# Kernel tuning notes

Hardware: AMD Instinct MI355X
Metric: run time of the kernel (lower is better)

The kernel has to match this reference:

```python
import jax, jax.numpy as jnp
import numpy as np
from jax import lax

STRIDE = 2
PADDING = 2
EPS = 1e-5


def _conv1d(x, w):
    # x: (N, C_in, T), w: (C_out, C_in, K) -> (N, C_out, T_out)
    return lax.conv_general_dilated(
        x, w, window_strides=(STRIDE,), padding=[(PADDING, PADDING)],
        dimension_numbers=("NCH", "OIH", "NCH"))


def setup_inputs() -> dict:
    key = jax.random.key(0)
    ks = jax.random.split(key, 5)
    Batch, num_sensors, in_c, out_c, k, T, r = 32, 8, 64, 128, 5, 2048, 8
    x = jax.random.normal(ks[0], (Batch * num_sensors, in_c, T), dtype=jnp.float32)
    A_flat = jax.random.normal(ks[1], (Batch, r * in_c * k), dtype=jnp.float32) * 0.02
    B_flat = jax.random.normal(ks[2], (Batch, out_c * r), dtype=jnp.float32) * 0.02
    fan_in = in_c * k
    conv_w = jax.random.normal(ks[3], (out_c, in_c, k), dtype=jnp.float32) / np.sqrt(fan_in)
    conv_b = jax.random.normal(ks[4], (out_c,), dtype=jnp.float32) * 0.01
    gamma = jnp.ones((out_c,), dtype=jnp.float32)
    beta = jnp.zeros((out_c,), dtype=jnp.float32)
    return {"x": x, "A_flat": A_flat, "B_flat": B_flat,
            "conv_w": conv_w, "conv_b": conv_b, "gamma": gamma, "beta": beta,
            "num_sensors": num_sensors, "r": r, "lora_scale": 0.5}


def reference(x, A_flat, B_flat, conv_w, conv_b, gamma, beta, num_sensors, r, lora_scale):
    Batch = A_flat.shape[0]
    out_c, in_c, k = conv_w.shape
    T = x.shape[-1]

    # base conv1d
    out_base = _conv1d(x, conv_w) + conv_b[None, :, None]  # (B*S, out_c, T_out)

    # dynamic per-sample LoRA delta weight: delta_W = B @ A, (Batch, out_c, in_c, k)
    A = A_flat.reshape(Batch, r, in_c * k)
    B_mat = B_flat.reshape(Batch, out_c, r)
    delta_W = jnp.einsum("bor,brm->bom", B_mat, A).reshape(Batch, out_c, in_c, k)
    delta_W = delta_W * lora_scale

    # per-sample conv: sensors of one sample share that sample's delta weight
    x_b = x.reshape(Batch, num_sensors, in_c, T)
    lora_out = jax.vmap(_conv1d)(x_b, delta_W)  # (Batch, S, out_c, T_out)
    lora_out = lora_out.reshape(Batch * num_sensors, out_c, -1)

    out = jax.nn.relu(out_base + lora_out)

    # GroupNorm, num_groups = min(4, out_c) reduced until divisible
    G = min(4, out_c)
    while out_c % G != 0:
        G -= 1
    N, C, To = out.shape
    og = out.reshape(N, G, C // G, To)
    mean = og.mean(axis=(2, 3), keepdims=True)
    var = og.var(axis=(2, 3), keepdims=True)
    normed = ((og - mean) * lax.rsqrt(var + EPS)).reshape(N, C, To)
    return normed * gamma[None, :, None] + beta[None, :, None]
```

## Files before the change

### kernel.cpp

```cpp
#include <hip/hip_runtime.h>
#include <hip/hip_bf16.h>

#define EPSV 1e-5f
#define PITCH 36
#define PCOLS 516

typedef short bf16x8 __attribute__((ext_vector_type(8)));
typedef short bf16x4 __attribute__((ext_vector_type(4)));
typedef float f32x4  __attribute__((ext_vector_type(4)));

__device__ __forceinline__ short f2bf(float f){
  unsigned u = __float_as_uint(f);
  u += 0x7fff + ((u >> 16) & 1);
  return (short)(u >> 16);
}
__device__ __forceinline__ int pk2(float a, float b){
  __hip_bfloat162 h = __float22bfloat162_rn(float2{a, b});
  return *reinterpret_cast<int*>(&h);
}

__global__ void build_weights(const float* __restrict__ A_flat,
                              const float* __restrict__ B_flat,
                              const float* __restrict__ conv_w,
                              const float* __restrict__ scale_p,
                              short* __restrict__ Wb){
  int idx = blockIdx.x * 256 + threadIdx.x;
  int ci = idx & 63;
  int co = (idx >> 6) & 127;
  int bj = idx >> 13;
  int b  = bj / 5;
  int j  = bj - 5 * b;
  int m  = ci * 5 + j;
  const float* Bp = B_flat + (b * 128 + co) * 8;
  const float* Ap = A_flat + b * 8 * 320 + m;
  float d = 0.f;
#pragma unroll
  for (int r = 0; r < 8; ++r) d = fmaf(Bp[r], Ap[r * 320], d);
  float w = conv_w[co * 320 + m] + scale_p[0] * d;
  Wb[idx] = f2bf(w);
}

__global__ __launch_bounds__(512, 4)
void conv_gn_mfma(const float* __restrict__ x,
                  const short* __restrict__ Wb,
                  const float* __restrict__ conv_b,
                  const float* __restrict__ gamma,
                  const float* __restrict__ beta,
                  float* __restrict__ out){
  __shared__ short xe[PCOLS * PITCH];
  __shared__ short xo[PCOLS * PITCH];
  __shared__ float redS[8], redQ[8], bc2[2];

  const int bid    = blockIdx.x;
  const int sample = ((bid & 7) << 5) + (bid >> 5);
  const int g      = (bid >> 3) & 3;
  const int b      = sample >> 3;
  const int tid    = threadIdx.x;
  const int lane   = tid & 63;
  const int wid    = tid >> 6;
  const int l16    = lane & 15;
  const int lk     = lane >> 4;

  f32x4 acc[2][8];
#pragma unroll
  for (int m2 = 0; m2 < 2; ++m2)
#pragma unroll
    for (int n = 0; n < 8; ++n) acc[m2][n] = (f32x4){0.f,0.f,0.f,0.f};

  const size_t wb_base = (size_t)b * 5 * 128 * 64;
  const float* xsamp = x + (size_t)sample * 64 * 2048;

#pragma unroll
  for (int ph = 0; ph < 4; ++ph) {
    const int th = ph >> 1;
    const int ch = ph & 1;

    if (ph) __syncthreads();
    {
      const float* xbase = xsamp + (size_t)(ch * 32) * 2048;
      const float* xr = xbase + (size_t)(wid * 4) * 2048 + th * 1024;
#pragma unroll 2
      for (int pass = 0; pass < 8; ++pass) {
        int c0 = pass * 128 + lane * 2;
        float2 v0 = *(const float2*)(xr + 0 * 2048 + c0);
        float2 v1 = *(const float2*)(xr + 1 * 2048 + c0);
        float2 v2 = *(const float2*)(xr + 2 * 2048 + c0);
        float2 v3 = *(const float2*)(xr + 3 * 2048 + c0);
        int pcol = pass * 64 + lane + 1;
        int2 ev = { pk2(v0.x, v1.x), pk2(v2.x, v3.x) };
        int2 od = { pk2(v0.y, v1.y), pk2(v2.y, v3.y) };
        *(int2*)(xe + pcol * PITCH + wid * 4) = ev;
        *(int2*)(xo + pcol * PITCH + wid * 4) = od;
      }
      if (tid < 128) {
        int which = tid >> 5;
        int ci    = tid & 31;
        int xc    = th * 1024 + ((which < 2) ? (which - 2) : (1024 + (which & 1)));
        float v = (xc >= 0 && xc < 2048) ? xbase[(size_t)ci * 2048 + xc] : 0.f;
        short* arr = (which & 1) ? xo : xe;
        arr[((which < 2) ? 0 : 513) * PITCH + ci] = f2bf(v);
      }
    }
    __syncthreads();
#pragma unroll
    for (int j = 0; j < 5; ++j) {
      const short* apb = Wb + wb_base + (size_t)(j * 128 + g * 32) * 64 + ch * 32 + lk * 8;
      bf16x8 a0 = *(const bf16x8*)(apb + (size_t)l16 * 64);
      bf16x8 a1 = *(const bf16x8*)(apb + (size_t)(l16 + 16) * 64);
      const short* arr = (j & 1) ? xo : xe;
      const int joff = (j & 1) ? ((j - 1) >> 1) : (j >> 1);
#pragma unroll
      for (int nn = 0; nn < 4; ++nn) {
        int tloc = wid * 64 + nn * 16 + l16;
        const short* bp = arr + (tloc + joff) * PITCH + lk * 8;
        bf16x4 lo = *(const bf16x4*)bp;
        bf16x4 hi = *(const bf16x4*)(bp + 4);
        bf16x8 bfr = {lo[0],lo[1],lo[2],lo[3],hi[0],hi[1],hi[2],hi[3]};
        const int n = th * 4 + nn;
        acc[0][n] = __builtin_amdgcn_mfma_f32_16x16x32_bf16(a0, bfr, acc[0][n], 0, 0, 0);
        acc[1][n] = __builtin_amdgcn_mfma_f32_16x16x32_bf16(a1, bfr, acc[1][n], 0, 0, 0);
      }
    }
  }

  float cb_[2][4], ga_[2][4], be_[2][4];
#pragma unroll
  for (int m2 = 0; m2 < 2; ++m2)
#pragma unroll
    for (int r = 0; r < 4; ++r) {
      int co = g * 32 + m2 * 16 + lk * 4 + r;
      cb_[m2][r] = conv_b[co];
      ga_[m2][r] = gamma[co];
      be_[m2][r] = beta[co];
    }
  float s1 = 0.f, s2 = 0.f;
#pragma unroll
  for (int m2 = 0; m2 < 2; ++m2)
#pragma unroll
    for (int n = 0; n < 8; ++n)
#pragma unroll
      for (int r = 0; r < 4; ++r) {
        float v = acc[m2][n][r] + cb_[m2][r];
        v = v > 0.f ? v : 0.f;
        acc[m2][n][r] = v;
        s1 += v;
        s2 = fmaf(v, v, s2);
      }
#pragma unroll
  for (int off = 32; off; off >>= 1) {
    s1 += __shfl_down(s1, off);
    s2 += __shfl_down(s2, off);
  }
  if (lane == 0) { redS[wid] = s1; redQ[wid] = s2; }
  __syncthreads();
  if (tid == 0) {
    float a = 0.f, q = 0.f;
#pragma unroll
    for (int w = 0; w < 8; ++w) { a += redS[w]; q += redQ[w]; }
    float mean = a * (1.f / 32768.f);
    float var  = q * (1.f / 32768.f) - mean * mean;
    bc2[0] = mean;
    bc2[1] = rsqrtf(var + EPSV);
  }
  __syncthreads();
  const float mean = bc2[0], inv = bc2[1];
  float* ob = out + (size_t)sample * 128 * 1024;
#pragma unroll
  for (int m2 = 0; m2 < 2; ++m2)
#pragma unroll
    for (int r = 0; r < 4; ++r) {
      int co = g * 32 + m2 * 16 + lk * 4 + r;
      float aa = ga_[m2][r] * inv;
      float bb = be_[m2][r] - mean * aa;
      float* orow = ob + (size_t)co * 1024 + l16;
#pragma unroll
      for (int n = 0; n < 8; ++n) {
        int t = (n >> 2) * 512 + wid * 64 + (n & 3) * 16;
        orow[t] = acc[m2][n][r] * aa + bb;
      }
    }
}

extern "C" void kernel_launch(void* const* d_in, const int* in_sizes, int n_in,
                              void* d_out, int out_size, void* d_ws, size_t ws_size,
                              hipStream_t stream) {
  const float* x       = (const float*)d_in[0];
  const float* A_flat  = (const float*)d_in[1];
  const float* B_flat  = (const float*)d_in[2];
  const float* conv_w  = (const float*)d_in[3];
  const float* conv_b  = (const float*)d_in[4];
  const float* gamma   = (const float*)d_in[5];
  const float* beta    = (const float*)d_in[6];
  const float* scale_p = (const float*)d_in[9];

  float* out = (float*)d_out;
  short* Wb  = (short*)d_ws;

  build_weights<<<5120, 256, 0, stream>>>(A_flat, B_flat, conv_w, scale_p, Wb);
  conv_gn_mfma<<<1024, 512, 0, stream>>>(x, Wb, conv_b, gamma, beta, out);
}
```

Before: 106.4 us.

## Give each wave a private LDS input tile and drop block barriers

The shared x staging buffers are split into per-wave tiles, each holding that wave's 64 output positions plus halo columns. Each wave now loads, converts and consumes its own slice, so the two `__syncthreads` per phase are removed and waves can run out of step with each other. The phase order is also swapped so the channel half is the outer loop. In exchange, each wave loads its halo columns again, and the LDS footprint grows slightly.

Result: slower. 111.5 us (+4.8%).

```diff
diff --git a/kernel.cpp b/kernel.cpp
--- a/kernel.cpp
+++ b/kernel.cpp
@@ -3,7 +3,8 @@
 
 #define EPSV 1e-5f
 #define PITCH 36
-#define PCOLS 516
+#define TILE_SH (66 * PITCH)
+#define WTILE_SH (2 * TILE_SH)
 
 typedef short bf16x8 __attribute__((ext_vector_type(8)));
 typedef short bf16x4 __attribute__((ext_vector_type(4)));
@@ -47,8 +48,7 @@
                   const float* __restrict__ gamma,
                   const float* __restrict__ beta,
                   float* __restrict__ out){
-  __shared__ short xe[PCOLS * PITCH];
-  __shared__ short xo[PCOLS * PITCH];
+  __shared__ short xt[8 * WTILE_SH];
   __shared__ float redS[8], redQ[8], bc2[2];
 
   const int bid    = blockIdx.x;
@@ -61,6 +61,9 @@
   const int l16    = lane & 15;
   const int lk     = lane >> 4;
 
+  short* xe = xt + wid * WTILE_SH;
+  short* xo = xe + TILE_SH;
+
   f32x4 acc[2][8];
 #pragma unroll
   for (int m2 = 0; m2 < 2; ++m2)
@@ -72,36 +75,40 @@
 
 #pragma unroll
   for (int ph = 0; ph < 4; ++ph) {
-    const int th = ph >> 1;
-    const int ch = ph & 1;
-
-    if (ph) __syncthreads();
+    const int ch = ph >> 1;
+    const int th = ph & 1;
+    const int T0 = th * 512 + wid * 64;
+
+    const float* xb = xsamp + (size_t)(ch * 32) * 2048;
+
     {
-      const float* xbase = xsamp + (size_t)(ch * 32) * 2048;
-      const float* xr = xbase + (size_t)(wid * 4) * 2048 + th * 1024;
-#pragma unroll 2
-      for (int pass = 0; pass < 8; ++pass) {
-        int c0 = pass * 128 + lane * 2;
-        float2 v0 = *(const float2*)(xr + 0 * 2048 + c0);
-        float2 v1 = *(const float2*)(xr + 1 * 2048 + c0);
-        float2 v2 = *(const float2*)(xr + 2 * 2048 + c0);
-        float2 v3 = *(const float2*)(xr + 3 * 2048 + c0);
-        int pcol = pass * 64 + lane + 1;
+      const int c = 2 * T0 + 2 * (int)lane;
+#pragma unroll
+      for (int rg = 0; rg < 8; ++rg) {
+        const float* r = xb + (size_t)(rg * 4) * 2048 + c;
+        float2 v0 = *(const float2*)(r);
+        float2 v1 = *(const float2*)(r + 2048);
+        float2 v2 = *(const float2*)(r + 4096);
+        float2 v3 = *(const float2*)(r + 6144);
         int2 ev = { pk2(v0.x, v1.x), pk2(v2.x, v3.x) };
         int2 od = { pk2(v0.y, v1.y), pk2(v2.y, v3.y) };
-        *(int2*)(xe + pcol * PITCH + wid * 4) = ev;
-        *(int2*)(xo + pcol * PITCH + wid * 4) = od;
-      }
-      if (tid < 128) {
-        int which = tid >> 5;
-        int ci    = tid & 31;
-        int xc    = th * 1024 + ((which < 2) ? (which - 2) : (1024 + (which & 1)));
-        float v = (xc >= 0 && xc < 2048) ? xbase[(size_t)ci * 2048 + xc] : 0.f;
-        short* arr = (which & 1) ? xo : xe;
-        arr[((which < 2) ? 0 : 513) * PITCH + ci] = f2bf(v);
-      }
-    }
-    __syncthreads();
+        *(int2*)(xe + (lane + 1) * PITCH + rg * 4) = ev;
+        *(int2*)(xo + (lane + 1) * PITCH + rg * 4) = od;
+      }
+      if (lane < 32) {
+        const int ci = lane;
+        float2 h{0.f, 0.f};
+        if (T0 > 0) h = *(const float2*)(xb + (size_t)ci * 2048 + (2 * T0 - 2));
+        xe[ci] = f2bf(h.x);
+        xo[ci] = f2bf(h.y);
+      } else {
+        const int ci = lane - 32;
+        const int xc = 2 * T0 + 128;
+        float v = (xc < 2048) ? xb[(size_t)ci * 2048 + xc] : 0.f;
+        xe[65 * PITCH + ci] = f2bf(v);
+      }
+    }
+
 #pragma unroll
     for (int j = 0; j < 5; ++j) {
       const short* apb = Wb + wb_base + (size_t)(j * 128 + g * 32) * 64 + ch * 32 + lk * 8;
@@ -111,8 +118,8 @@
       const int joff = (j & 1) ? ((j - 1) >> 1) : (j >> 1);
 #pragma unroll
       for (int nn = 0; nn < 4; ++nn) {
-        int tloc = wid * 64 + nn * 16 + l16;
-        const short* bp = arr + (tloc + joff) * PITCH + lk * 8;
+        int tl = nn * 16 + l16;
+        const short* bp = arr + (tl + joff) * PITCH + lk * 8;
         bf16x4 lo = *(const bf16x4*)bp;
         bf16x4 hi = *(const bf16x4*)(bp + 4);
         bf16x8 bfr = {lo[0],lo[1],lo[2],lo[3],hi[0],hi[1],hi[2],hi[3]};
```

## Double-buffer x tiles in LDS and compute two GroupNorm groups per block

Applied to the files above, without the earlier changes.

Each block now handles 64 output channels (two GroupNorm groups) rather than 32, which halves the grid and halves the number of times each sample's input is loaded and converted. The LDS staging buffer is now double-buffered, and loading of the next phase's x chunk is interleaved with the MFMA work on the current chunk, using registers as a prefetch stage. This aims to hide global-load latency and remove redundant x traffic. The cost is roughly twice the accumulator registers and LDS per block, with occupancy lowered to 2 blocks per CU and only 512 blocks launched.

Result: slower. 112.9 us (+6.1%).

```diff
diff --git a/kernel.cpp b/kernel.cpp
--- a/kernel.cpp
+++ b/kernel.cpp
@@ -40,20 +40,21 @@
   Wb[idx] = f2bf(w);
 }
 
-__global__ __launch_bounds__(512, 4)
+__global__ __launch_bounds__(512, 2)
 void conv_gn_mfma(const float* __restrict__ x,
                   const short* __restrict__ Wb,
                   const float* __restrict__ conv_b,
                   const float* __restrict__ gamma,
                   const float* __restrict__ beta,
                   float* __restrict__ out){
-  __shared__ short xe[PCOLS * PITCH];
-  __shared__ short xo[PCOLS * PITCH];
-  __shared__ float redS[8], redQ[8], bc2[2];
+  __shared__ short xbuf[2][2][PCOLS * PITCH];
+  __shared__ float redS[2][8], redQ[2][8], bcv[4];
 
   const int bid    = blockIdx.x;
-  const int sample = ((bid & 7) << 5) + (bid >> 5);
-  const int g      = (bid >> 3) & 3;
+  const int xcd    = bid & 7;
+  const int u      = bid >> 3;
+  const int sample = xcd * 32 + (u >> 1);
+  const int h      = u & 1;
   const int b      = sample >> 3;
   const int tid    = threadIdx.x;
   const int lane   = tid & 63;
@@ -61,81 +62,150 @@
   const int l16    = lane & 15;
   const int lk     = lane >> 4;
 
-  f32x4 acc[2][8];
-#pragma unroll
-  for (int m2 = 0; m2 < 2; ++m2)
+  f32x4 acc[4][8];
+#pragma unroll
+  for (int m2 = 0; m2 < 4; ++m2)
 #pragma unroll
     for (int n = 0; n < 8; ++n) acc[m2][n] = (f32x4){0.f,0.f,0.f,0.f};
 
   const size_t wb_base = (size_t)b * 5 * 128 * 64;
   const float* xsamp = x + (size_t)sample * 64 * 2048;
+  const int hwhich = tid >> 5, hci = tid & 31;
+
+  {
+    const float* xr = xsamp + (size_t)(wid * 4) * 2048;
+    short* xe = xbuf[0][0];
+    short* xo = xbuf[0][1];
+#pragma unroll
+    for (int pass = 0; pass < 8; ++pass) {
+      int c0 = pass * 128 + lane * 2;
+      float2 v0 = *(const float2*)(xr + c0);
+      float2 v1 = *(const float2*)(xr + c0 + 2048);
+      float2 v2 = *(const float2*)(xr + c0 + 4096);
+      float2 v3 = *(const float2*)(xr + c0 + 6144);
+      int2 ev = { pk2(v0.x, v1.x), pk2(v2.x, v3.x) };
+      int2 od = { pk2(v0.y, v1.y), pk2(v2.y, v3.y) };
+      *(int2*)(xe + (pass * 64 + lane + 1) * PITCH + wid * 4) = ev;
+      *(int2*)(xo + (pass * 64 + lane + 1) * PITCH + wid * 4) = od;
+    }
+    if (tid < 128) {
+      int xc = (hwhich < 2) ? (hwhich - 2) : (1024 + (hwhich & 1));
+      float v = (xc >= 0 && xc < 2048) ? xsamp[(size_t)hci * 2048 + xc] : 0.f;
+      short* arr = (hwhich & 1) ? xo : xe;
+      arr[((hwhich < 2) ? 0 : 513) * PITCH + hci] = f2bf(v);
+    }
+  }
+  __syncthreads();
+
+#define COMPUTE_J(J, TH, CH, XE, XO)                                            \
+  {                                                                             \
+    const short* arr = ((J) & 1) ? (XO) : (XE);                                 \
+    const int joff = ((J) & 1) ? (((J) - 1) >> 1) : ((J) >> 1);                 \
+    const short* apb = Wb + wb_base + (size_t)((J) * 128 + h * 64) * 64         \
+                          + (CH) * 32 + lk * 8;                                 \
+    bf16x8 a0 = *(const bf16x8*)(apb + (size_t)(l16)      * 64);                \
+    bf16x8 a1 = *(const bf16x8*)(apb + (size_t)(l16 + 16) * 64);                \
+    bf16x8 a2 = *(const bf16x8*)(apb + (size_t)(l16 + 32) * 64);                \
+    bf16x8 a3 = *(const bf16x8*)(apb + (size_t)(l16 + 48) * 64);                \
+    _Pragma("unroll")                                                           \
+    for (int nn = 0; nn < 4; ++nn) {                                            \
+      int tl = wid * 64 + nn * 16 + l16;                                        \
+      const short* bp = arr + (tl + joff) * PITCH + lk * 8;                     \
+      bf16x4 lo = *(const bf16x4*)bp;                                           \
+      bf16x4 hi = *(const bf16x4*)(bp + 4);                                     \
+      bf16x8 bfr = {lo[0],lo[1],lo[2],lo[3],hi[0],hi[1],hi[2],hi[3]};           \
+      const int n = (TH) * 4 + nn;                                              \
+      acc[0][n] = __builtin_amdgcn_mfma_f32_16x16x32_bf16(a0, bfr, acc[0][n], 0,0,0); \
+      acc[1][n] = __builtin_amdgcn_mfma_f32_16x16x32_bf16(a1, bfr, acc[1][n], 0,0,0); \
+      acc[2][n] = __builtin_amdgcn_mfma_f32_16x16x32_bf16(a2, bfr, acc[2][n], 0,0,0); \
+      acc[3][n] = __builtin_amdgcn_mfma_f32_16x16x32_bf16(a3, bfr, acc[3][n], 0,0,0); \
+    }                                                                           \
+  }
+
+  float2 pf[16];
+  float hv = 0.f;
 
 #pragma unroll
   for (int ph = 0; ph < 4; ++ph) {
-    const int th = ph >> 1;
-    const int ch = ph & 1;
-
-    if (ph) __syncthreads();
-    {
-      const float* xbase = xsamp + (size_t)(ch * 32) * 2048;
-      const float* xr = xbase + (size_t)(wid * 4) * 2048 + th * 1024;
-#pragma unroll 2
-      for (int pass = 0; pass < 8; ++pass) {
+    const int th = ph >> 1, ch = ph & 1;
+    short* xe = xbuf[ph & 1][0];
+    short* xo = xbuf[ph & 1][1];
+    const int nth = (ph + 1) >> 1, nch = (ph + 1) & 1;
+    const float* nxb = xsamp + (size_t)(nch * 32) * 2048;
+    const float* nxr = nxb + (size_t)(wid * 4) * 2048 + nth * 1024;
+    short* nxe = xbuf[(ph + 1) & 1][0];
+    short* nxo = xbuf[(ph + 1) & 1][1];
+
+    if (ph < 3) {
+#pragma unroll
+      for (int pass = 0; pass < 4; ++pass) {
         int c0 = pass * 128 + lane * 2;
-        float2 v0 = *(const float2*)(xr + 0 * 2048 + c0);
-        float2 v1 = *(const float2*)(xr + 1 * 2048 + c0);
-        float2 v2 = *(const float2*)(xr + 2 * 2048 + c0);
-        float2 v3 = *(const float2*)(xr + 3 * 2048 + c0);
-        int pcol = pass * 64 + lane + 1;
-        int2 ev = { pk2(v0.x, v1.x), pk2(v2.x, v3.x) };
-        int2 od = { pk2(v0.y, v1.y), pk2(v2.y, v3.y) };
-        *(int2*)(xe + pcol * PITCH + wid * 4) = ev;
-        *(int2*)(xo + pcol * PITCH + wid * 4) = od;
+        pf[pass*4+0] = *(const float2*)(nxr + c0);
+        pf[pass*4+1] = *(const float2*)(nxr + c0 + 2048);
+        pf[pass*4+2] = *(const float2*)(nxr + c0 + 4096);
+        pf[pass*4+3] = *(const float2*)(nxr + c0 + 6144);
       }
       if (tid < 128) {
-        int which = tid >> 5;
-        int ci    = tid & 31;
-        int xc    = th * 1024 + ((which < 2) ? (which - 2) : (1024 + (which & 1)));
-        float v = (xc >= 0 && xc < 2048) ? xbase[(size_t)ci * 2048 + xc] : 0.f;
-        short* arr = (which & 1) ? xo : xe;
-        arr[((which < 2) ? 0 : 513) * PITCH + ci] = f2bf(v);
+        int xc = nth * 1024 + ((hwhich < 2) ? (hwhich - 2) : (1024 + (hwhich & 1)));
+        hv = (xc >= 0 && xc < 2048) ? nxb[(size_t)hci * 2048 + xc] : 0.f;
+      }
+    }
+
+    COMPUTE_J(0, th, ch, xe, xo)
+    COMPUTE_J(1, th, ch, xe, xo)
+    COMPUTE_J(2, th, ch, xe, xo)
+
+    if (ph < 3) {
+#pragma unroll
+      for (int pass = 0; pass < 4; ++pass) {
+        int2 ev = { pk2(pf[pass*4+0].x, pf[pass*4+1].x), pk2(pf[pass*4+2].x, pf[pass*4+3].x) };
+        int2 od = { pk2(pf[pass*4+0].y, pf[pass*4+1].y), pk2(pf[pass*4+2].y, pf[pass*4+3].y) };
+        *(int2*)(nxe + (pass * 64 + lane + 1) * PITCH + wid * 4) = ev;
+        *(int2*)(nxo + (pass * 64 + lane + 1) * PITCH + wid * 4) = od;
+      }
+      if (tid < 128) {
+        short* arr = (hwhich & 1) ? nxo : nxe;
+        arr[((hwhich < 2) ? 0 : 513) * PITCH + hci] = f2bf(hv);
+      }
+#pragma unroll
+      for (int pass = 4; pass < 8; ++pass) {
+        int c0 = pass * 128 + lane * 2;
+        pf[(pass-4)*4+0] = *(const float2*)(nxr + c0);
+        pf[(pass-4)*4+1] = *(const float2*)(nxr + c0 + 2048);
+        pf[(pass-4)*4+2] = *(const float2*)(nxr + c0 + 4096);
+        pf[(pass-4)*4+3] = *(const float2*)(nxr + c0 + 6144);
+      }
+    }
+
+    COMPUTE_J(3, th, ch, xe, xo)
+    COMPUTE_J(4, th, ch, xe, xo)
+
+    if (ph < 3) {
+#pragma unroll
+      for (int pass = 4; pass < 8; ++pass) {
+        int2 ev = { pk2(pf[(pass-4)*4+0].x, pf[(pass-4)*4+1].x), pk2(pf[(pass-4)*4+2].x, pf[(pass-4)*4+3].x) };
+        int2 od = { pk2(pf[(pass-4)*4+0].y, pf[(pass-4)*4+1].y), pk2(pf[(pass-4)*4+2].y, pf[(pass-4)*4+3].y) };
+        *(int2*)(nxe + (pass * 64 + lane + 1) * PITCH + wid * 4) = ev;
+        *(int2*)(nxo + (pass * 64 + lane + 1) * PITCH + wid * 4) = od;
       }
     }
     __syncthreads();
-#pragma unroll
-    for (int j = 0; j < 5; ++j) {
-      const short* apb = Wb + wb_base + (size_t)(j * 128 + g * 32) * 64 + ch * 32 + lk * 8;
-      bf16x8 a0 = *(const bf16x8*)(apb + (size_t)l16 * 64);
-      bf16x8 a1 = *(const bf16x8*)(apb + (size_t)(l16 + 16) * 64);
-      const short* arr = (j & 1) ? xo : xe;
-      const int joff = (j & 1) ? ((j - 1) >> 1) : (j >> 1);
-#pragma unroll
-      for (int nn = 0; nn < 4; ++nn) {
-        int tloc = wid * 64 + nn * 16 + l16;
-        const short* bp = arr + (tloc + joff) * PITCH + lk * 8;
-        bf16x4 lo = *(const bf16x4*)bp;
-        bf16x4 hi = *(const bf16x4*)(bp + 4);
-        bf16x8 bfr = {lo[0],lo[1],lo[2],lo[3],hi[0],hi[1],hi[2],hi[3]};
-        const int n = th * 4 + nn;
-        acc[0][n] = __builtin_amdgcn_mfma_f32_16x16x32_bf16(a0, bfr, acc[0][n], 0, 0, 0);
-        acc[1][n] = __builtin_amdgcn_mfma_f32_16x16x32_bf16(a1, bfr, acc[1][n], 0, 0, 0);
-      }
-    }
-  }
-
-  float cb_[2][4], ga_[2][4], be_[2][4];
-#pragma unroll
-  for (int m2 = 0; m2 < 2; ++m2)
+  }
+
+  float cb_[4][4], ga_[4][4], be_[4][4];
+#pragma unroll
+  for (int m2 = 0; m2 < 4; ++m2)
 #pragma unroll
     for (int r = 0; r < 4; ++r) {
-      int co = g * 32 + m2 * 16 + lk * 4 + r;
+      int co = h * 64 + m2 * 16 + lk * 4 + r;
       cb_[m2][r] = conv_b[co];
       ga_[m2][r] = gamma[co];
       be_[m2][r] = beta[co];
     }
-  float s1 = 0.f, s2 = 0.f;
-#pragma unroll
-  for (int m2 = 0; m2 < 2; ++m2)
+  float s1[2] = {0.f, 0.f}, s2[2] = {0.f, 0.f};
+#pragma unroll
+  for (int m2 = 0; m2 < 4; ++m2) {
+    const int grp = m2 >> 1;
 #pragma unroll
     for (int n = 0; n < 8; ++n)
 #pragma unroll
@@ -143,33 +213,40 @@
         float v = acc[m2][n][r] + cb_[m2][r];
         v = v > 0.f ? v : 0.f;
         acc[m2][n][r] = v;
-        s1 += v;
-        s2 = fmaf(v, v, s2);
-      }
+        s1[grp] += v;
+        s2[grp] = fmaf(v, v, s2[grp]);
+      }
+  }
 #pragma unroll
   for (int off = 32; off; off >>= 1) {
-    s1 += __shfl_down(s1, off);
-    s2 += __shfl_down(s2, off);
-  }
-  if (lane == 0) { redS[wid] = s1; redQ[wid] = s2; }
+    s1[0] += __shfl_down(s1[0], off);
+    s2[0] += __shfl_down(s2[0], off);
+    s1[1] += __shfl_down(s1[1], off);
+    s2[1] += __shfl_down(s2[1], off);
+  }
+  if (lane == 0) {
+    redS[0][wid] = s1[0]; redQ[0][wid] = s2[0];
+    redS[1][wid] = s1[1]; redQ[1][wid] = s2[1];
+  }
   __syncthreads();
-  if (tid == 0) {
+  if (tid < 2) {
     float a = 0.f, q = 0.f;
 #pragma unroll
-    for (int w = 0; w < 8; ++w) { a += redS[w]; q += redQ[w]; }
+    for (int w = 0; w < 8; ++w) { a += redS[tid][w]; q += redQ[tid][w]; }
     float mean = a * (1.f / 32768.f);
     float var  = q * (1.f / 32768.f) - mean * mean;
-    bc2[0] = mean;
-    bc2[1] = rsqrtf(var + EPSV);
+    bcv[tid * 2]     = mean;
+    bcv[tid * 2 + 1] = rsqrtf(var + EPSV);
   }
   __syncthreads();
-  const float mean = bc2[0], inv = bc2[1];
   float* ob = out + (size_t)sample * 128 * 1024;
 #pragma unroll
-  for (int m2 = 0; m2 < 2; ++m2)
+  for (int m2 = 0; m2 < 4; ++m2) {
+    const float mean = bcv[(m2 >> 1) * 2];
+    const float inv  = bcv[(m2 >> 1) * 2 + 1];
 #pragma unroll
     for (int r = 0; r < 4; ++r) {
-      int co = g * 32 + m2 * 16 + lk * 4 + r;
+      int co = h * 64 + m2 * 16 + lk * 4 + r;
       float aa = ga_[m2][r] * inv;
       float bb = be_[m2][r] - mean * aa;
       float* orow = ob + (size_t)co * 1024 + l16;
@@ -179,6 +256,7 @@
         orow[t] = acc[m2][n][r] * aa + bb;
       }
     }
+  }
 }
 
 extern "C" void kernel_launch(void* const* d_in, const int* in_sizes, int n_in,
@@ -197,5 +275,5 @@
   short* Wb  = (short*)d_ws;
 
   build_weights<<<5120, 256, 0, stream>>>(A_flat, B_flat, conv_w, scale_p, Wb);
-  conv_gn_mfma<<<1024, 512, 0, stream>>>(x, Wb, conv_b, gamma, beta, out);
-}
+  conv_gn_mfma<<<512, 512, 0, stream>>>(x, Wb, conv_b, gamma, beta, out);
+}
```

## Prefetch x tile with float4 loads into registers and repack the LDS layout

Applied to the files above, without the earlier changes.

The x staging loop now issues sixteen float4 global loads per thread up front, holding them in registers, before packing to bf16 and writing even and odd columns into one merged LDS buffer. The LDS pitch drops from 36 to 34 shorts to change the bank mapping, and the halo load shrinks to the three halo columns that are actually read. The phase order now iterates channel half outer and time half inner. Launch bounds are relaxed to two blocks per CU so the extra prefetch registers fit. The risks are that 64-bit LDS accesses at the 68-byte pitch become misaligned, and that register pressure rises.

Measured after the change: 207.2 us. 1.95x slower.

```diff
diff --git a/kernel.cpp b/kernel.cpp
--- a/kernel.cpp
+++ b/kernel.cpp
@@ -2,8 +2,9 @@
 #include <hip/hip_bf16.h>
 
 #define EPSV 1e-5f
-#define PITCH 36
+#define PITCH 34
 #define PCOLS 516
+#define PARSZ (PCOLS * PITCH)
 
 typedef short bf16x8 __attribute__((ext_vector_type(8)));
 typedef short bf16x4 __attribute__((ext_vector_type(4)));
@@ -40,15 +41,14 @@
   Wb[idx] = f2bf(w);
 }
 
-__global__ __launch_bounds__(512, 4)
+__global__ __launch_bounds__(512, 2)
 void conv_gn_mfma(const float* __restrict__ x,
                   const short* __restrict__ Wb,
                   const float* __restrict__ conv_b,
                   const float* __restrict__ gamma,
                   const float* __restrict__ beta,
                   float* __restrict__ out){
-  __shared__ short xe[PCOLS * PITCH];
-  __shared__ short xo[PCOLS * PITCH];
+  __shared__ short xls[2 * PARSZ];
   __shared__ float redS[8], redQ[8], bc2[2];
 
   const int bid    = blockIdx.x;
@@ -69,50 +69,56 @@
 
   const size_t wb_base = (size_t)b * 5 * 128 * 64;
   const float* xsamp = x + (size_t)sample * 64 * 2048;
+  const int hw_ = tid >> 5, hci = tid & 31;
 
 #pragma unroll
   for (int ph = 0; ph < 4; ++ph) {
-    const int th = ph >> 1;
-    const int ch = ph & 1;
-
+    const int ch = ph >> 1;
+    const int th = ph & 1;
     if (ph) __syncthreads();
+
     {
-      const float* xbase = xsamp + (size_t)(ch * 32) * 2048;
-      const float* xr = xbase + (size_t)(wid * 4) * 2048 + th * 1024;
-#pragma unroll 2
-      for (int pass = 0; pass < 8; ++pass) {
-        int c0 = pass * 128 + lane * 2;
-        float2 v0 = *(const float2*)(xr + 0 * 2048 + c0);
-        float2 v1 = *(const float2*)(xr + 1 * 2048 + c0);
-        float2 v2 = *(const float2*)(xr + 2 * 2048 + c0);
-        float2 v3 = *(const float2*)(xr + 3 * 2048 + c0);
-        int pcol = pass * 64 + lane + 1;
-        int2 ev = { pk2(v0.x, v1.x), pk2(v2.x, v3.x) };
-        int2 od = { pk2(v0.y, v1.y), pk2(v2.y, v3.y) };
-        *(int2*)(xe + pcol * PITCH + wid * 4) = ev;
-        *(int2*)(xo + pcol * PITCH + wid * 4) = od;
-      }
-      if (tid < 128) {
-        int which = tid >> 5;
-        int ci    = tid & 31;
-        int xc    = th * 1024 + ((which < 2) ? (which - 2) : (1024 + (which & 1)));
-        float v = (xc >= 0 && xc < 2048) ? xbase[(size_t)ci * 2048 + xc] : 0.f;
-        short* arr = (which & 1) ? xo : xe;
-        arr[((which < 2) ? 0 : 513) * PITCH + ci] = f2bf(v);
+      const float* xr = xsamp + (size_t)(ch * 32 + wid * 4) * 2048 + th * 1024;
+      float4 pf[16];
+#pragma unroll
+      for (int p = 0; p < 4; ++p)
+#pragma unroll
+        for (int r = 0; r < 4; ++r)
+          pf[p*4 + r] = *(const float4*)(xr + (size_t)r * 2048 + p * 256 + lane * 4);
+
+      float hv = 0.f;
+      if (tid < 96) {
+        int xc = th * 1024 + (hw_ == 0 ? -2 : hw_ == 1 ? -1 : 1024);
+        if (xc >= 0 && xc < 2048) hv = xsamp[(size_t)(ch * 32 + hci) * 2048 + xc];
+      }
+
+#pragma unroll
+      for (int p = 0; p < 4; ++p) {
+        float4 v0 = pf[p*4+0], v1 = pf[p*4+1], v2 = pf[p*4+2], v3 = pf[p*4+3];
+        const int pe = p * 128 + 2 * (int)lane + 1;
+        *(int2*)&xls[ pe      * PITCH + wid * 4] = int2{pk2(v0.x, v1.x), pk2(v2.x, v3.x)};
+        *(int2*)&xls[(pe + 1) * PITCH + wid * 4] = int2{pk2(v0.z, v1.z), pk2(v2.z, v3.z)};
+        *(int2*)&xls[PARSZ +  pe      * PITCH + wid * 4] = int2{pk2(v0.y, v1.y), pk2(v2.y, v3.y)};
+        *(int2*)&xls[PARSZ + (pe + 1) * PITCH + wid * 4] = int2{pk2(v0.w, v1.w), pk2(v2.w, v3.w)};
+      }
+      if (tid < 96) {
+        int prow = (hw_ == 2) ? 513 : 0;
+        xls[(hw_ == 1 ? PARSZ : 0) + prow * PITCH + hci] = f2bf(hv);
       }
     }
     __syncthreads();
+
 #pragma unroll
     for (int j = 0; j < 5; ++j) {
       const short* apb = Wb + wb_base + (size_t)(j * 128 + g * 32) * 64 + ch * 32 + lk * 8;
       bf16x8 a0 = *(const bf16x8*)(apb + (size_t)l16 * 64);
       bf16x8 a1 = *(const bf16x8*)(apb + (size_t)(l16 + 16) * 64);
-      const short* arr = (j & 1) ? xo : xe;
-      const int joff = (j & 1) ? ((j - 1) >> 1) : (j >> 1);
+      const short* arr = xls + ((j & 1) ? PARSZ : 0);
+      const int joff = j >> 1;
 #pragma unroll
       for (int nn = 0; nn < 4; ++nn) {
-        int tloc = wid * 64 + nn * 16 + l16;
-        const short* bp = arr + (tloc + joff) * PITCH + lk * 8;
+        int pcol = wid * 64 + nn * 16 + l16 + joff;
+        const short* bp = arr + pcol * PITCH + lk * 8;
         bf16x4 lo = *(const bf16x4*)bp;
         bf16x4 hi = *(const bf16x4*)(bp + 4);
         bf16x8 bfr = {lo[0],lo[1],lo[2],lo[3],hi[0],hi[1],hi[2],hi[3]};
```
